# Kernel optimization log

Measured on AMD Instinct MI355X. Metric: run time of the kernel, lower is better.

Reference implementation:

```python
import jax, jax.numpy as jnp
import numpy as np

B, T, C = 4, 2048, 1024
H = 16  # NUM_HEADS
HD = C // H  # head_dim = 64


def setup_inputs() -> dict:
    key = jax.random.key(0)
    k1, k2, k3 = jax.random.split(key, 3)
    x = jax.random.normal(k1, (B, T, C), dtype=jnp.float32)
    # nn.Linear weights: stored as [out, in]; apply as x @ W.T
    W_attn = jax.random.normal(k2, (3 * C, C), dtype=jnp.float32) * (1.0 / np.sqrt(C))
    W_proj = jax.random.normal(k3, (C, C), dtype=jnp.float32) * (1.0 / np.sqrt(C))
    return {"x": x, "W_attn": W_attn, "W_proj": W_proj}


def reference(x, W_attn, W_proj):
    Bv, Tv, Cv = x.shape
    qkv = x @ W_attn.T  # [B, T, 3C]
    q, k, v = jnp.split(qkv, 3, axis=2)
    # [B, H, T, HD]
    q = q.reshape(Bv, Tv, H, HD).transpose(0, 2, 1, 3)
    k = k.reshape(Bv, Tv, H, HD).transpose(0, 2, 1, 3)
    v = v.reshape(Bv, Tv, H, HD).transpose(0, 2, 1, 3)
    att = jnp.einsum("bhqd,bhkd->bhqk", q, k) * (1.0 / np.sqrt(HD))
    causal = jnp.tril(jnp.ones((Tv, Tv), dtype=bool))
    att = jnp.where(causal[None, None, :, :], att, -jnp.inf)
    att = jax.nn.softmax(att, axis=-1)
    y = jnp.einsum("bhqk,bhkd->bhqd", att, v)
    y = y.transpose(0, 2, 1, 3).reshape(Bv, Tv, Cv)
    return y @ W_proj.T
```

## Files before the change

### kernel.cpp

```cpp
#include <hip/hip_runtime.h>

typedef _Float16 f16;
typedef _Float16 half8 __attribute__((ext_vector_type(8)));
typedef _Float16 half4v __attribute__((ext_vector_type(4)));
typedef __fp16 fp16x2 __attribute__((ext_vector_type(2)));
typedef float floatx4 __attribute__((ext_vector_type(4)));
typedef unsigned int uint;

constexpr int Bsz = 4, Tseq = 2048, Cdim = 1024, NH = 16, HDim = 64;
constexpr int Mtok = Bsz * Tseq;
constexpr int NQT = Tseq / 64;
constexpr float QSCALE = 0.18033688f;

#define GLDS16(src, dst) __builtin_amdgcn_global_load_lds( \
    (const __attribute__((address_space(1))) void*)(src),  \
    (__attribute__((address_space(3))) void*)(dst), 16, 0, 0)

__device__ __forceinline__ float fexp2(float x) { return __builtin_amdgcn_exp2f(x); }
__device__ __forceinline__ uint pkrtz(float a, float b) {
  fp16x2 h = __builtin_amdgcn_cvt_pkrtz(a, b);
  return __builtin_bit_cast(uint, h);
}
#define MFMA16(a, b, c) __builtin_amdgcn_mfma_f32_16x16x32_f16((a), (b), (c), 0, 0, 0)

__global__ void cvt3_kernel(const float* __restrict__ x, const float* __restrict__ wa,
                            const float* __restrict__ wp,
                            f16* __restrict__ xh, f16* __restrict__ wah, f16* __restrict__ wph) {
  constexpr int nx = Mtok * Cdim, nwa = 3 * Cdim * Cdim, nwp = Cdim * Cdim;
  int i = (blockIdx.x * blockDim.x + threadIdx.x) * 4;
  const float* src; f16* dst; int off;
  if (i < nx)            { src = x;  dst = xh;  off = i; }
  else if (i < nx + nwa) { src = wa; dst = wah; off = i - nx; }
  else                   { src = wp; dst = wph; off = i - nx - nwa; }
  float4 v = *(const float4*)(src + off);
  half4v o;
  o[0] = (f16)v.x; o[1] = (f16)v.y; o[2] = (f16)v.z; o[3] = (f16)v.w;
  *(half4v*)(dst + off) = o;
}

__global__ __launch_bounds__(512, 2)
void qk8p_kernel(const f16* __restrict__ X, const f16* __restrict__ W,
                 f16* __restrict__ q_out, f16* __restrict__ k_out)
{
  __shared__ __align__(16) char smem[131072];
  constexpr int K = 1024, NT = 16;
  const int sbid = (blockIdx.x & 7) * 32 + (blockIdx.x >> 3);
  const int bm = sbid >> 3, bn = sbid & 7;
  const int m0 = bm * 256, n0 = bn * 256;
  const int tid = threadIdx.x, w = tid >> 6, lane = tid & 63;
  const int wr = w >> 2, wc = w & 3;
  const int g = lane >> 4, lm = lane & 15;

  const int grow = lane >> 3;
  const int cg = (lane & 7) ^ grow;

  auto stage_half = [&](int op, int t, int h) {
    const f16* src = op ? W : X;
    char* base = smem + op * 65536 + (t & 1) * 32768 + h * 16384;
    const int rbase = (op ? n0 : m0) + h * 128;
#pragma unroll
    for (int r2 = 0; r2 < 2; ++r2) {
      int row = rbase + r2 * 64 + w * 8 + grow;
      GLDS16(src + (size_t)row * K + t * 64 + cg * 8,
             base + (r2 * 64 + w * 8) * 128);
    }
  };

  floatx4 acc[8][4];
#pragma unroll
  for (int i = 0; i < 8; ++i)
#pragma unroll
    for (int j = 0; j < 4; ++j) acc[i][j] = (floatx4)0.0f;

  const int sw = lm & 7;
  const char* S = smem;
  const int Abase = wr * 16384 + lm * 128;
  const int Bbase = 65536 + (wc >> 1) * 16384 + ((wc & 1) * 64 + lm) * 128;

  half8 a0[4][2], a1[4][2], b0[2][2], b1[2][2];

  stage_half(0, 0, 0); stage_half(0, 0, 1);
  stage_half(1, 0, 0); stage_half(1, 0, 1);
  stage_half(1, 1, 0); stage_half(1, 1, 1);

#pragma unroll 2
  for (int t = 0; t < NT; ++t) {
    const int par = (t & 1) * 32768;

    if (t == NT - 1) { asm volatile("s_waitcnt vmcnt(0)" ::: "memory"); }
    else             { asm volatile("s_waitcnt vmcnt(4)" ::: "memory"); }
    __builtin_amdgcn_s_barrier();
#pragma unroll
    for (int i = 0; i < 4; ++i)
#pragma unroll
      for (int kk = 0; kk < 2; ++kk)
        a0[i][kk] = *(const half8*)(S + par + Abase + i * 2048 + 16 * ((kk * 4 + g) ^ sw));
#pragma unroll
    for (int j = 0; j < 2; ++j)
#pragma unroll
      for (int kk = 0; kk < 2; ++kk)
        b0[j][kk] = *(const half8*)(S + par + Bbase + j * 2048 + 16 * ((kk * 4 + g) ^ sw));
    if (t + 1 < NT) stage_half(0, t + 1, 0);
    asm volatile("s_waitcnt lgkmcnt(0)" ::: "memory");
    __builtin_amdgcn_sched_barrier(0);
    __builtin_amdgcn_s_setprio(1);
#pragma unroll
    for (int i = 0; i < 4; ++i)
#pragma unroll
      for (int j = 0; j < 2; ++j)
#pragma unroll
        for (int kk = 0; kk < 2; ++kk)
          acc[i][j] = MFMA16(a0[i][kk], b0[j][kk], acc[i][j]);
    __builtin_amdgcn_s_setprio(0);

    __builtin_amdgcn_s_barrier();
#pragma unroll
    for (int j = 0; j < 2; ++j)
#pragma unroll
      for (int kk = 0; kk < 2; ++kk)
        b1[j][kk] = *(const half8*)(S + par + Bbase + (j + 2) * 2048 + 16 * ((kk * 4 + g) ^ sw));
    if (t + 1 < NT) stage_half(0, t + 1, 1);
    asm volatile("s_waitcnt lgkmcnt(0)" ::: "memory");
    __builtin_amdgcn_sched_barrier(0);
    __builtin_amdgcn_s_setprio(1);
#pragma unroll
    for (int i = 0; i < 4; ++i)
#pragma unroll
      for (int j = 0; j < 2; ++j)
#pragma unroll
        for (int kk = 0; kk < 2; ++kk)
          acc[i][j + 2] = MFMA16(a0[i][kk], b1[j][kk], acc[i][j + 2]);
    __builtin_amdgcn_s_setprio(0);

    __builtin_amdgcn_s_barrier();
#pragma unroll
    for (int i = 0; i < 4; ++i)
#pragma unroll
      for (int kk = 0; kk < 2; ++kk)
        a1[i][kk] = *(const half8*)(S + par + Abase + (i + 4) * 2048 + 16 * ((kk * 4 + g) ^ sw));
    if (t + 2 < NT) stage_half(1, t + 2, 0);
    asm volatile("s_waitcnt lgkmcnt(0)" ::: "memory");
    __builtin_amdgcn_sched_barrier(0);
    __builtin_amdgcn_s_setprio(1);
#pragma unroll
    for (int i = 0; i < 4; ++i)
#pragma unroll
      for (int j = 0; j < 2; ++j)
#pragma unroll
        for (int kk = 0; kk < 2; ++kk)
          acc[i + 4][j + 2] = MFMA16(a1[i][kk], b1[j][kk], acc[i + 4][j + 2]);
    __builtin_amdgcn_s_setprio(0);

    __builtin_amdgcn_s_barrier();
    if (t + 2 < NT) stage_half(1, t + 2, 1);
    __builtin_amdgcn_s_setprio(1);
#pragma unroll
    for (int i = 0; i < 4; ++i)
#pragma unroll
      for (int j = 0; j < 2; ++j)
#pragma unroll
        for (int kk = 0; kk < 2; ++kk)
          acc[i + 4][j] = MFMA16(a1[i][kk], b0[j][kk], acc[i + 4][j]);
    __builtin_amdgcn_s_setprio(0);
  }

#pragma unroll
  for (int i = 0; i < 8; ++i) {
#pragma unroll
    for (int j = 0; j < 4; ++j) {
#pragma unroll
      for (int r = 0; r < 4; ++r) {
        int m = m0 + wr * 128 + i * 16 + 4 * g + r;
        int n = n0 + wc * 64 + j * 16 + lm;
        float v = acc[i][j][r];
        int which = n >> 10;
        int inner = n & 1023;
        int h = inner >> 6, hd = inner & 63;
        int b = m >> 11, t = m & 2047;
        if (which == 0) {
          v *= QSCALE;
          q_out[(((size_t)(b * NH + h)) * Tseq + t) * HDim + hd] = (f16)v;
        } else {
          k_out[(((size_t)(b * NH + h)) * Tseq + t) * HDim + hd] = (f16)v;
        }
      }
    }
  }
}

template<int EPI>
__device__ __forceinline__ void g8p_body(char* smem,
    const f16* __restrict__ A, const f16* __restrict__ B,
    float* __restrict__ outF, f16* __restrict__ v_out,
    int bm, int bn)
{
  constexpr int K = 1024, NT = 16;
  const int m0 = bm * 128, n0 = bn * 256;
  const int tid = threadIdx.x, w = tid >> 6, lane = tid & 63;
  const int wr = w >> 2, wc = w & 3;
  const int g = lane >> 4, lm = lane & 15;
  const int grow = lane >> 3;
  const int cg = (lane & 7) ^ grow;

  auto stage_A = [&](int t, int h) {
    int row = m0 + h * 64 + w * 8 + grow;
    GLDS16(A + (size_t)row * K + t * 64 + cg * 8,
           smem + (t & 1) * 16384 + (h * 64 + w * 8) * 128);
  };
  auto stage_B = [&](int t, int h) {
#pragma unroll
    for (int r2 = 0; r2 < 2; ++r2) {
      int row = n0 + h * 128 + r2 * 64 + w * 8 + grow;
      GLDS16(B + (size_t)row * K + t * 64 + cg * 8,
             smem + 32768 + (t & 1) * 32768 + (h * 128 + r2 * 64 + w * 8) * 128);
    }
  };

  floatx4 acc[4][4];
#pragma unroll
  for (int i = 0; i < 4; ++i)
#pragma unroll
    for (int j = 0; j < 4; ++j) acc[i][j] = (floatx4)0.0f;

  const int sw = lm & 7;
  const char* S = smem;
  const int Abase = (wr * 64 + lm) * 128;
  const int Bbase = 32768 + (wc * 64 + lm) * 128;

  half8 a0[2][2], a1[2][2], b0[2][2], b1[2][2];

  stage_A(0, 0); stage_A(0, 1);
  stage_B(0, 0); stage_B(0, 1);
  stage_B(1, 0); stage_B(1, 1);

#pragma unroll 2
  for (int t = 0; t < NT; ++t) {
    const int parA = (t & 1) * 16384;
    const int parB = (t & 1) * 32768;

    if (t == NT - 1) { asm volatile("s_waitcnt vmcnt(0)" ::: "memory"); }
    else             { asm volatile("s_waitcnt vmcnt(4)" ::: "memory"); }
    __builtin_amdgcn_s_barrier();
#pragma unroll
    for (int i = 0; i < 2; ++i)
#pragma unroll
      for (int kk = 0; kk < 2; ++kk)
        a0[i][kk] = *(const half8*)(S + parA + Abase + i * 2048 + 16 * ((kk * 4 + g) ^ sw));
#pragma unroll
    for (int j = 0; j < 2; ++j)
#pragma unroll
      for (int kk = 0; kk < 2; ++kk)
        b0[j][kk] = *(const half8*)(S + parB + Bbase + j * 2048 + 16 * ((kk * 4 + g) ^ sw));
    if (t + 1 < NT) stage_A(t + 1, 0);
    asm volatile("s_waitcnt lgkmcnt(0)" ::: "memory");
    __builtin_amdgcn_sched_barrier(0);
    __builtin_amdgcn_s_setprio(1);
#pragma unroll
    for (int i = 0; i < 2; ++i)
#pragma unroll
      for (int j = 0; j < 2; ++j)
#pragma unroll
        for (int kk = 0; kk < 2; ++kk)
          acc[i][j] = MFMA16(a0[i][kk], b0[j][kk], acc[i][j]);
    __builtin_amdgcn_s_setprio(0);

    __builtin_amdgcn_s_barrier();
#pragma unroll
    for (int j = 0; j < 2; ++j)
#pragma unroll
      for (int kk = 0; kk < 2; ++kk)
        b1[j][kk] = *(const half8*)(S + parB + Bbase + (j + 2) * 2048 + 16 * ((kk * 4 + g) ^ sw));
    if (t + 1 < NT) stage_A(t + 1, 1);
    asm volatile("s_waitcnt lgkmcnt(0)" ::: "memory");
    __builtin_amdgcn_sched_barrier(0);
    __builtin_amdgcn_s_setprio(1);
#pragma unroll
    for (int i = 0; i < 2; ++i)
#pragma unroll
      for (int j = 0; j < 2; ++j)
#pragma unroll
        for (int kk = 0; kk < 2; ++kk)
          acc[i][j + 2] = MFMA16(a0[i][kk], b1[j][kk], acc[i][j + 2]);
    __builtin_amdgcn_s_setprio(0);

    __builtin_amdgcn_s_barrier();
#pragma unroll
    for (int i = 0; i < 2; ++i)
#pragma unroll
      for (int kk = 0; kk < 2; ++kk)
        a1[i][kk] = *(const half8*)(S + parA + Abase + (i + 2) * 2048 + 16 * ((kk * 4 + g) ^ sw));
    if (t + 2 < NT) stage_B(t + 2, 0);
    asm volatile("s_waitcnt lgkmcnt(0)" ::: "memory");
    __builtin_amdgcn_sched_barrier(0);
    __builtin_amdgcn_s_setprio(1);
#pragma unroll
    for (int i = 0; i < 2; ++i)
#pragma unroll
      for (int j = 0; j < 2; ++j)
#pragma unroll
        for (int kk = 0; kk < 2; ++kk)
          acc[i + 2][j + 2] = MFMA16(a1[i][kk], b1[j][kk], acc[i + 2][j + 2]);
    __builtin_amdgcn_s_setprio(0);

    __builtin_amdgcn_s_barrier();
    if (t + 2 < NT) stage_B(t + 2, 1);
    __builtin_amdgcn_s_setprio(1);
#pragma unroll
    for (int i = 0; i < 2; ++i)
#pragma unroll
      for (int j = 0; j < 2; ++j)
#pragma unroll
        for (int kk = 0; kk < 2; ++kk)
          acc[i + 2][j] = MFMA16(a1[i][kk], b0[j][kk], acc[i + 2][j]);
    __builtin_amdgcn_s_setprio(0);
  }

#pragma unroll
  for (int i = 0; i < 4; ++i) {
#pragma unroll
    for (int j = 0; j < 4; ++j) {
#pragma unroll
      for (int r = 0; r < 4; ++r) {
        int m = m0 + wr * 64 + i * 16 + 4 * g + r;
        int n = n0 + wc * 64 + j * 16 + lm;
        float v = acc[i][j][r];
        if constexpr (EPI == 1) {
          outF[(size_t)m * Cdim + n] = v;
        } else {
          int h = m >> 6, hd = m & 63;
          int b = n >> 11, tt = n & 2047;
          v_out[(((size_t)(b * NH + h)) * HDim + hd) * Tseq + tt] = (f16)v;
        }
      }
    }
  }
}

__global__ __launch_bounds__(512, 2)
void vt8p_kernel(const f16* __restrict__ xh, const f16* __restrict__ wVh, f16* __restrict__ Vth) {
  __shared__ __align__(16) char smem[98304];
  const int x = blockIdx.x & 7, q = blockIdx.x >> 3;
  int bn = x * 4 + (q >> 3);
  int bm = q & 7;
  g8p_body<2>(smem, wVh, xh, nullptr, Vth, bm, bn);
}

__global__ __launch_bounds__(512, 2)
void proj8p_kernel(const f16* __restrict__ yh, const f16* __restrict__ wPh, float* __restrict__ out) {
  __shared__ __align__(16) char smem[98304];
  const int x = blockIdx.x & 7, q = blockIdx.x >> 3;
  int bm = x * 8 + (q >> 2);
  int bn = q & 3;
  g8p_body<1>(smem, yh, wPh, out, nullptr, bm, bn);
}

__device__ __forceinline__ void softmax_tile(floatx4* s,
                                             bool diag, int j0, int qg, char* pwrow, int g, int lm) {
  if (diag) {
#pragma unroll
    for (int nf = 0; nf < 4; ++nf)
#pragma unroll
      for (int r = 0; r < 4; ++r)
        if (j0 + nf * 16 + 4 * g + r > qg) s[nf][r] = -1e30f;
  }
#pragma unroll
  for (int nf = 0; nf < 4; ++nf) {
    float p0 = fexp2(s[nf][0]), p1 = fexp2(s[nf][1]);
    float p2 = fexp2(s[nf][2]), p3 = fexp2(s[nf][3]);
    uint lo = pkrtz(p0, p1), hi = pkrtz(p2, p3);
    int slot = 2 * nf + (g >> 1);
    uint2 u; u.x = lo; u.y = hi;
    *(uint2*)(pwrow + 16 * (slot ^ (lm & 7)) + 8 * (g & 1)) = u;
  }
}

__device__ __forceinline__ void store_o(const floatx4* acc, const floatx4 l5, int q0w,
                                        int g, int lm, f16* __restrict__ Y, int b, int h) {
#pragma unroll
  for (int r = 0; r < 4; ++r) {
    float inv = 1.0f / l5[r];
    int t = q0w + 4 * g + r;
    size_t base = ((size_t)(b * Tseq + t)) * Cdim + h * HDim;
#pragma unroll
    for (int ng = 0; ng < 4; ++ng)
      Y[base + ng * 16 + lm] = (f16)(acc[ng][r] * inv);
  }
}

__global__ __launch_bounds__(256)
void attn_kernel(const f16* __restrict__ Q, const f16* __restrict__ Kg,
                 const f16* __restrict__ Vt, f16* __restrict__ Y)
{
  __shared__ __align__(16) char smem[40960];
  int wg = blockIdx.x;
  int lin = (wg & 7) * 128 + (wg >> 3);
  const int p  = lin & 15;
  const int bh = lin >> 4;
  const int itB = NQT - p;
  const f16* Qb  = Q  + (size_t)bh * Tseq * HDim;
  const f16* Kb  = Kg + (size_t)bh * Tseq * HDim;
  const f16* Vtb = Vt + (size_t)bh * HDim * Tseq;

  const int tid = threadIdx.x, w = tid >> 6, lane = tid & 63;
  const int g = lane >> 4, lm = lane & 15;
  char* pwrow = smem + 32768 + w * 2048 + lm * 128;
  const int b = bh >> 4, h = bh & 15;

  half8 ones;
#pragma unroll
  for (int i = 0; i < 8; ++i) ones[i] = (f16)1.0f;

  int q0 = (NQT - 1 - p) * 64;
  int qg = q0 + w * 16 + lm;
  half8 qf0 = *(const half8*)(Qb + (size_t)(q0 + w * 16 + lm) * HDim + g * 8);
  half8 qf1 = *(const half8*)(Qb + (size_t)(q0 + w * 16 + lm) * HDim + 32 + g * 8);

  floatx4 acc[4], acc5;
  acc5 = (floatx4)0.f;
#pragma unroll
  for (int ng = 0; ng < 4; ++ng) acc[ng] = (floatx4)0.f;

  const int srow = w * 8 + (lane >> 3);
  const int sslot = lane & 7;

  auto stage = [&](int j0s, int buf) {
#pragma unroll
    for (int t = 0; t < 2; ++t) {
      int row = srow + t * 32;
      int cg = sslot ^ (row & 7);
      GLDS16(Kb + (size_t)(j0s + row) * HDim + cg * 8,
             smem + buf * 8192 + (w * 8 + t * 32) * 128);
      GLDS16(Vtb + (size_t)row * Tseq + j0s + cg * 8,
             smem + 16384 + buf * 8192 + (w * 8 + t * 32) * 128);
    }
  };

  stage(0, 0);
  asm volatile("s_waitcnt vmcnt(0)" ::: "memory");
  __builtin_amdgcn_s_barrier();

  for (int it = 0; it < NQT + 1; ++it) {
    const bool lastB = (it == itB - 1);
    const bool last  = (it == NQT);
    const int jt = (it < itB) ? it : it - itB;
    const int j0 = jt * 64;

    if (!last) {
      const int itn = it + 1;
      const int jtn = (itn < itB) ? itn : itn - itB;
      stage(jtn * 64, itn & 1);
    }

    char* kb   = smem + (it & 1) * 8192;
    char* vbuf = smem + 16384 + (it & 1) * 8192;

    floatx4 s[4];
    __builtin_amdgcn_s_setprio(1);
#pragma unroll
    for (int nf = 0; nf < 4; ++nf) {
      half8 kf0 = *(const half8*)(kb + (nf * 16 + lm) * 128 + 16 * ((g)     ^ (lm & 7)));
      half8 kf1 = *(const half8*)(kb + (nf * 16 + lm) * 128 + 16 * ((4 + g) ^ (lm & 7)));
      s[nf] = MFMA16(kf0, qf0, (floatx4)0.f);
      s[nf] = MFMA16(kf1, qf1, s[nf]);
    }
    __builtin_amdgcn_s_setprio(0);

    softmax_tile(s, lastB || last, j0, qg, pwrow, g, lm);
    half8 pa0 = *(const half8*)(pwrow + 16 * ((g)     ^ (lm & 7)));
    half8 pa1 = *(const half8*)(pwrow + 16 * ((4 + g) ^ (lm & 7)));

    __builtin_amdgcn_s_setprio(1);
    acc5 = MFMA16(pa0, ones, acc5);
    acc5 = MFMA16(pa1, ones, acc5);
#pragma unroll
    for (int c = 0; c < 2; ++c)
#pragma unroll
      for (int ng = 0; ng < 4; ++ng) {
        half8 vbf = *(const half8*)(vbuf + (ng * 16 + lm) * 128 + 16 * ((4 * c + g) ^ (lm & 7)));
        acc[ng] = MFMA16(c ? pa1 : pa0, vbf, acc[ng]);
      }
    __builtin_amdgcn_s_setprio(0);

    asm volatile("s_waitcnt vmcnt(0)" ::: "memory");
    __builtin_amdgcn_s_barrier();

    if (lastB) {
      store_o(acc, acc5, q0 + 16 * w, g, lm, Y, b, h);
      q0 = p * 64;
      qg = q0 + w * 16 + lm;
      qf0 = *(const half8*)(Qb + (size_t)(q0 + w * 16 + lm) * HDim + g * 8);
      qf1 = *(const half8*)(Qb + (size_t)(q0 + w * 16 + lm) * HDim + 32 + g * 8);
      acc5 = (floatx4)0.f;
#pragma unroll
      for (int ng = 0; ng < 4; ++ng) acc[ng] = (floatx4)0.f;
    }
  }

  store_o(acc, acc5, q0 + 16 * w, g, lm, Y, b, h);
}

extern "C" void kernel_launch(void* const* d_in, const int* in_sizes, int n_in,
                              void* d_out, int out_size, void* d_ws, size_t ws_size,
                              hipStream_t stream)
{
  const float* x      = (const float*)d_in[0];
  const float* W_attn = (const float*)d_in[1];
  const float* W_proj = (const float*)d_in[2];
  float* out = (float*)d_out;

  char* ws = (char*)d_ws;
  f16* xh  = (f16*)(ws);
  f16* wAh = (f16*)(ws + (size_t)(16u << 20));
  f16* wPh = (f16*)(ws + (size_t)(22u << 20));
  f16* Qh  = (f16*)(ws + (size_t)(24u << 20));
  f16* Kh  = (f16*)(ws + (size_t)(40u << 20));
  f16* Vth = (f16*)(ws + (size_t)(56u << 20));
  f16* yh  = xh;

  constexpr int ntot = (Mtok * Cdim + 3 * Cdim * Cdim + Cdim * Cdim) / 4;
  cvt3_kernel<<<(ntot + 255) / 256, 256, 0, stream>>>(x, W_attn, W_proj, xh, wAh, wPh);

  qk8p_kernel<<<dim3(256), 512, 0, stream>>>(xh, wAh, Qh, Kh);

  vt8p_kernel<<<dim3(256), 512, 0, stream>>>(xh, wAh + (size_t)2048 * Cdim, Vth);

  attn_kernel<<<dim3(1024), 256, 0, stream>>>(Qh, Kh, Vth, yh);

  proj8p_kernel<<<dim3(256), 512, 0, stream>>>(yh, wPh, out);
}
```

Measured before the change: 155.2 us.

## Merge QK and V-transpose GEMMs into one launch; split attention loop by phase

```diff
diff --git a/kernel.cpp b/kernel.cpp
--- a/kernel.cpp
+++ b/kernel.cpp
@@ -38,13 +38,11 @@
   *(half4v*)(dst + off) = o;
 }
 
-__global__ __launch_bounds__(512, 2)
-void qk8p_kernel(const f16* __restrict__ X, const f16* __restrict__ W,
-                 f16* __restrict__ q_out, f16* __restrict__ k_out)
+__device__ __forceinline__ void qk8p_body(char* smem,
+    const f16* __restrict__ X, const f16* __restrict__ W,
+    f16* __restrict__ q_out, f16* __restrict__ k_out, int sbid)
 {
-  __shared__ __align__(16) char smem[131072];
   constexpr int K = 1024, NT = 16;
-  const int sbid = (blockIdx.x & 7) * 32 + (blockIdx.x >> 3);
   const int bm = sbid >> 3, bn = sbid & 7;
   const int m0 = bm * 256, n0 = bn * 256;
   const int tid = threadIdx.x, w = tid >> 6, lane = tid & 63;
@@ -337,12 +335,19 @@
 }
 
 __global__ __launch_bounds__(512, 2)
-void vt8p_kernel(const f16* __restrict__ xh, const f16* __restrict__ wVh, f16* __restrict__ Vth) {
-  __shared__ __align__(16) char smem[98304];
-  const int x = blockIdx.x & 7, q = blockIdx.x >> 3;
-  int bn = x * 4 + (q >> 3);
-  int bm = q & 7;
-  g8p_body<2>(smem, wVh, xh, nullptr, Vth, bm, bn);
+void qkvt_kernel(const f16* __restrict__ xh, const f16* __restrict__ wAh,
+                 f16* __restrict__ Qh, f16* __restrict__ Kh, f16* __restrict__ Vth) {
+  __shared__ __align__(16) char smem[131072];
+  if (blockIdx.x < 256) {
+    int sbid = (blockIdx.x & 7) * 32 + (blockIdx.x >> 3);
+    qk8p_body(smem, xh, wAh, Qh, Kh, sbid);
+  } else {
+    int bx = blockIdx.x - 256;
+    int x = bx & 7, q = bx >> 3;
+    int bn = x * 4 + (q >> 3);
+    int bm = q & 7;
+    g8p_body<2>(smem, wAh + (size_t)2048 * Cdim, xh, nullptr, Vth, bm, bn);
+  }
 }
 
 __global__ __launch_bounds__(512, 2)
@@ -435,25 +440,9 @@
     }
   };
 
-  stage(0, 0);
-  asm volatile("s_waitcnt vmcnt(0)" ::: "memory");
-  __builtin_amdgcn_s_barrier();
-
-  for (int it = 0; it < NQT + 1; ++it) {
-    const bool lastB = (it == itB - 1);
-    const bool last  = (it == NQT);
-    const int jt = (it < itB) ? it : it - itB;
-    const int j0 = jt * 64;
-
-    if (!last) {
-      const int itn = it + 1;
-      const int jtn = (itn < itB) ? itn : itn - itB;
-      stage(jtn * 64, itn & 1);
-    }
-
-    char* kb   = smem + (it & 1) * 8192;
-    char* vbuf = smem + 16384 + (it & 1) * 8192;
-
+  auto compute = [&](int j0, int par, bool diag) {
+    char* kb   = smem + par * 8192;
+    char* vbuf = smem + 16384 + par * 8192;
     floatx4 s[4];
     __builtin_amdgcn_s_setprio(1);
 #pragma unroll
@@ -465,7 +454,7 @@
     }
     __builtin_amdgcn_s_setprio(0);
 
-    softmax_tile(s, lastB || last, j0, qg, pwrow, g, lm);
+    softmax_tile(s, diag, j0, qg, pwrow, g, lm);
     half8 pa0 = *(const half8*)(pwrow + 16 * ((g)     ^ (lm & 7)));
     half8 pa1 = *(const half8*)(pwrow + 16 * ((4 + g) ^ (lm & 7)));
 
@@ -480,21 +469,41 @@
         acc[ng] = MFMA16(c ? pa1 : pa0, vbf, acc[ng]);
       }
     __builtin_amdgcn_s_setprio(0);
-
+  };
+
+  stage(0, 0);
+  asm volatile("s_waitcnt vmcnt(0)" ::: "memory");
+  __builtin_amdgcn_s_barrier();
+
+  int git = 0;
+  for (int jt = 0; jt < itB - 1; ++jt, ++git) {
+    stage((jt + 1) * 64, (git + 1) & 1);
+    compute(jt * 64, git & 1, false);
     asm volatile("s_waitcnt vmcnt(0)" ::: "memory");
     __builtin_amdgcn_s_barrier();
-
-    if (lastB) {
-      store_o(acc, acc5, q0 + 16 * w, g, lm, Y, b, h);
-      q0 = p * 64;
-      qg = q0 + w * 16 + lm;
-      qf0 = *(const half8*)(Qb + (size_t)(q0 + w * 16 + lm) * HDim + g * 8);
-      qf1 = *(const half8*)(Qb + (size_t)(q0 + w * 16 + lm) * HDim + 32 + g * 8);
-      acc5 = (floatx4)0.f;
-#pragma unroll
-      for (int ng = 0; ng < 4; ++ng) acc[ng] = (floatx4)0.f;
-    }
-  }
+  }
+  stage(0, (git + 1) & 1);
+  compute((itB - 1) * 64, git & 1, true);
+  asm volatile("s_waitcnt vmcnt(0)" ::: "memory");
+  __builtin_amdgcn_s_barrier();
+  ++git;
+
+  store_o(acc, acc5, q0 + 16 * w, g, lm, Y, b, h);
+  q0 = p * 64;
+  qg = q0 + w * 16 + lm;
+  qf0 = *(const half8*)(Qb + (size_t)(q0 + w * 16 + lm) * HDim + g * 8);
+  qf1 = *(const half8*)(Qb + (size_t)(q0 + w * 16 + lm) * HDim + 32 + g * 8);
+  acc5 = (floatx4)0.f;
+#pragma unroll
+  for (int ng = 0; ng < 4; ++ng) acc[ng] = (floatx4)0.f;
+
+  for (int jt = 0; jt < p; ++jt, ++git) {
+    stage((jt + 1) * 64, (git + 1) & 1);
+    compute(jt * 64, git & 1, false);
+    asm volatile("s_waitcnt vmcnt(0)" ::: "memory");
+    __builtin_amdgcn_s_barrier();
+  }
+  compute(p * 64, git & 1, true);
 
   store_o(acc, acc5, q0 + 16 * w, g, lm, Y, b, h);
 }
@@ -520,9 +529,7 @@
   constexpr int ntot = (Mtok * Cdim + 3 * Cdim * Cdim + Cdim * Cdim) / 4;
   cvt3_kernel<<<(ntot + 255) / 256, 256, 0, stream>>>(x, W_attn, W_proj, xh, wAh, wPh);
 
-  qk8p_kernel<<<dim3(256), 512, 0, stream>>>(xh, wAh, Qh, Kh);
-
-  vt8p_kernel<<<dim3(256), 512, 0, stream>>>(xh, wAh + (size_t)2048 * Cdim, Vth);
+  qkvt_kernel<<<dim3(512), 512, 0, stream>>>(xh, wAh, Qh, Kh, Vth);
 
   attn_kernel<<<dim3(1024), 256, 0, stream>>>(Qh, Kh, Vth, yh);
 
```

Measured after the change: 153.7 us. About the same (-1.0%).
